# Performance work log

Hardware: AMD Instinct MI355X
Metric: run time of the kernel (lower is better)

The kernel has to match this reference:

```python
import jax, jax.numpy as jnp
import numpy as np

EPS = 1e-12  # torch F.normalize default eps


def conv1x1(x, w, b):
    # x: [N,C,H,W], w: [K,C], b: [K]
    return jnp.einsum('nchw,kc->nkhw', x, w) + b[None, :, None, None]


def forward_sa(f1, f2, cw1, cb1, cw2, cb2):
    n, _, h, w = f1.shape
    c1 = conv1x1(f1, cw1, cb1)  # [N,1,H,W]
    c2 = conv1x1(f2, cw2, cb2)
    c1 = jax.nn.softmax(c1.reshape(n, h * w), axis=1).reshape(n, 1, h, w)
    c2 = jax.nn.softmax(c2.reshape(n, h * w), axis=1).reshape(n, 1, h, w)
    return c1 * f1, c2 * f2


def l2norm_ch(x):
    # torch F.normalize(x) -> p=2 over dim=1 with eps clamp
    n = jnp.sqrt(jnp.sum(x * x, axis=1, keepdims=True))
    return x / jnp.maximum(n, EPS)


def forward_ca(f1, f2, pw1, pb1, pw2, pb2):
    N, C, H, W = f1.shape
    f1_cl = conv1x1(f1, pw1, pb1).reshape(N, -1, H * W)  # [N,Cl,HW]
    f2_cl = conv1x1(f2, pw2, pb2).reshape(N, -1, H * W)
    # A[n,p,q] = sum_c f2_cl[n,c,p] * f1_cl[n,c,q]  -> [N,HW,HW]
    A_c = jnp.tanh(jnp.einsum('ncp,ncq->npq', f2_cl, f1_cl))
    f1_v = f1.reshape(N, C, H * W)
    f2_v = f2.reshape(N, C, H * W)
    # f1_hat = f1_v @ A_c^T ; f2_hat = f2_v @ A_c
    f1_hat = jnp.einsum('ncp,nqp->ncq', f1_v, A_c).reshape(N, C, H, W)
    f2_hat = jnp.einsum('ncp,npq->ncq', f2_v, A_c).reshape(N, C, H, W)
    return l2norm_ch(f1_hat), l2norm_ch(f2_hat)


def setup_inputs() -> dict:
    key = jax.random.key(0)
    ks = jax.random.split(key, 10)
    N, C, H, W = 2, 256, 64, 64
    Cl = C // 16
    sc = 1.0 / np.sqrt(C)
    return {
        'f1': jax.random.normal(ks[0], (N, C, H, W), jnp.float32),
        'f2': jax.random.normal(ks[1], (N, C, H, W), jnp.float32),
        'pw1': jax.random.normal(ks[2], (Cl, C), jnp.float32) * sc,
        'pb1': jax.random.normal(ks[3], (Cl,), jnp.float32) * sc,
        'pw2': jax.random.normal(ks[4], (Cl, C), jnp.float32) * sc,
        'pb2': jax.random.normal(ks[5], (Cl,), jnp.float32) * sc,
        'cw1': jax.random.normal(ks[6], (1, C), jnp.float32) * sc,
        'cb1': jax.random.normal(ks[7], (1,), jnp.float32) * sc,
        'cw2': jax.random.normal(ks[8], (1, C), jnp.float32) * sc,
        'cb2': jax.random.normal(ks[9], (1,), jnp.float32) * sc,
    }


def reference(f1, f2, pw1, pb1, pw2, pb2, cw1, cb1, cw2, cb2):
    f1_1, f2_1 = forward_sa(f1, f2, cw1, cb1, cw2, cb2)
    f1_hat, f2_hat = forward_ca(f1_1, f2_1, pw1, pb1, pw2, pb2)
    fp1_hat = jax.nn.relu(f1_hat + f1)
    fp2_hat = jax.nn.relu(f2_hat + f2)
    f1_2, f2_2 = forward_sa(fp1_hat, fp2_hat, cw1, cb1, cw2, cb2)
    # Original calls forward_ca(f1_2, f2_2) again but discards the result
    # and returns (f1_2, f2_2); the dead call is omitted (identical output).
    return (f1_2, f2_2)
```

## Files before the change

kernel.cpp:

```cpp
#include <hip/hip_runtime.h>
#include <hip/hip_bf16.h>
#include <math.h>

#define N_B 2
#define C_CH 256
#define HW_SZ 4096
#define CL_CH 16

typedef __bf16 bf16x8 __attribute__((ext_vector_type(8)));
typedef float f32x4 __attribute__((ext_vector_type(4)));
typedef float f32x16 __attribute__((ext_vector_type(16)));

__device__ __forceinline__ unsigned short f2bf(float x){
  __hip_bfloat16 b = __float2bfloat16(x);
  return *reinterpret_cast<unsigned short*>(&b);
}
__device__ __forceinline__ float bf2f(unsigned short u){
  unsigned int w = ((unsigned int)u) << 16;
  return *reinterpret_cast<float*>(&w);
}
__device__ __forceinline__ unsigned int cvtpk(float a, float b){
  unsigned int r;
  asm("v_cvt_pk_bf16_f32 %0, %1, %2" : "=v"(r) : "v"(a), "v"(b));
  return r;
}
__device__ __forceinline__ float tanh_fast(float x){
  float e = __expf(2.0f * x);
  return fmaf(-2.0f, __builtin_amdgcn_rcpf(1.0f + e), 1.0f);
}
__device__ __forceinline__ void gload16(const void* gsrc, void* lds_dst){
  __builtin_amdgcn_global_load_lds(
      (const __attribute__((address_space(1))) unsigned int*)gsrc,
      (__attribute__((address_space(3))) unsigned int*)lds_dst, 16, 0, 0);
}

__global__ void k_conv1(const float* __restrict__ f1, const float* __restrict__ f2,
                        const float* __restrict__ w1, const float* __restrict__ w2,
                        const float* __restrict__ b1, const float* __restrict__ b2,
                        float* __restrict__ cv){
  const int i = blockIdx.z, n = blockIdx.y, t = threadIdx.x;
  const int ql = t & 63, cg = t >> 6;
  const int q = blockIdx.x * 64 + ql;
  const float* f = (i ? f2 : f1) + n * C_CH * HW_SZ;
  const float* w = i ? w2 : w1;
  __shared__ float ws[C_CH];
  __shared__ float red[4][72];
  ws[t] = w[t];
  __syncthreads();
  float acc = 0.f;
  #pragma unroll 8
  for (int c = cg * 64; c < cg * 64 + 64; ++c)
    acc += f[c * HW_SZ + q] * ws[c];
  red[cg][ql] = acc;
  __syncthreads();
  if (t < 64){
    float s = red[0][t] + red[1][t] + red[2][t] + red[3][t] + (i ? b2[0] : b1[0]);
    cv[(i * 2 + n) * HW_SZ + blockIdx.x * 64 + t] = s;
  }
}

__global__ void k_scale_cl(const float* __restrict__ f1, const float* __restrict__ f2,
                           const float* __restrict__ cv,
                           const float* __restrict__ pw1, const float* __restrict__ pw2,
                           const float* __restrict__ pb1, const float* __restrict__ pb2,
                           unsigned short* __restrict__ fs1, unsigned short* __restrict__ fs2,
                           unsigned short* __restrict__ clT1, unsigned short* __restrict__ clT2){
  const int i = blockIdx.z, n = blockIdx.y, t = threadIdx.x;
  const int ql = t & 63, cg = t >> 6;
  const int q = blockIdx.x * 64 + ql;
  const float* f = (i ? f2 : f1) + n * C_CH * HW_SZ;
  unsigned short* fs = (i ? fs2 : fs1) + n * C_CH * HW_SZ;
  unsigned short* clT = (i ? clT2 : clT1) + n * 32 * HW_SZ;
  const float* pw = i ? pw2 : pw1;
  const float* pb = i ? pb2 : pb1;
  const float* cvrow = cv + (i * 2 + n) * HW_SZ;
  __shared__ float wls[CL_CH * C_CH];
  __shared__ float red[4][CL_CH][66];
  __shared__ float smr[256];
  #pragma unroll
  for (int j = 0; j < 16; j++) wls[j * 256 + t] = pw[j * 256 + t];
  float sv[16];
  float m = -1e30f;
  #pragma unroll
  for (int j = 0; j < 16; j++){ sv[j] = cvrow[j * 256 + t]; m = fmaxf(m, sv[j]); }
  smr[t] = m; __syncthreads();
  for (int s = 128; s > 0; s >>= 1){ if (t < s) smr[t] = fmaxf(smr[t], smr[t + s]); __syncthreads(); }
  m = smr[0]; __syncthreads();
  float sum = 0.f;
  #pragma unroll
  for (int j = 0; j < 16; j++) sum += __expf(sv[j] - m);
  smr[t] = sum; __syncthreads();
  for (int s = 128; s > 0; s >>= 1){ if (t < s) smr[t] += smr[t + s]; __syncthreads(); }
  const float p = __expf(cvrow[q] - m) * (1.0f / smr[0]);

  float acc[16];
  #pragma unroll
  for (int k = 0; k < 16; k++) acc[k] = 0.f;
  for (int c = cg * 64; c < cg * 64 + 64; ++c){
    float vv = f[c * HW_SZ + q] * p;
    fs[c * HW_SZ + q] = f2bf(vv);
    #pragma unroll
    for (int k = 0; k < 16; k++) acc[k] += wls[k * 256 + c] * vv;
  }
  #pragma unroll
  for (int k = 0; k < 16; k++) red[cg][k][ql] = acc[k];
  __syncthreads();
  #pragma unroll
  for (int j = 0; j < 4; j++){
    int e = j * 256 + t; int k = e >> 6, qq = e & 63;
    float s = red[0][k][qq] + red[1][k][qq] + red[2][k][qq] + red[3][k][qq] + pb[k];
    clT[(blockIdx.x * 64 + qq) * 32 + k] = f2bf(s);
  }
  if (t < 128){
    uint4 zv = {0u, 0u, 0u, 0u};
    int qq = t >> 1, half = t & 1;
    *reinterpret_cast<uint4*>(&clT[(blockIdx.x * 64 + qq) * 32 + 16 + half * 8]) = zv;
  }
}

__global__ __launch_bounds__(512, 2) void k_hat(
    const unsigned short* __restrict__ fs1, const unsigned short* __restrict__ fs2,
    const unsigned short* __restrict__ clT1, const unsigned short* __restrict__ clT2,
    float* __restrict__ hat1, float* __restrict__ hat2,
    float* __restrict__ pt1, float* __restrict__ pt2){
  const int t = threadIdx.x;
  const int bid = blockIdx.x;
  const int xcd = bid & 7, slot = bid >> 3;
  const int z = xcd >> 1;
  const int n = z & 1, i = z >> 1;
  const int x = slot * 2 + (xcd & 1);
  const int qt = x >> 1, ph = x & 1;
  const int q0 = qt * 128;
  const int pbase = ph * 2048;

  const unsigned short* fs = (i ? fs2 : fs1) + n * C_CH * HW_SZ;
  const unsigned short* uT = (i ? clT1 : clT2) + n * 32 * HW_SZ;
  const unsigned short* vT = (i ? clT2 : clT1) + n * 32 * HW_SZ;
  float* out = (ph ? (i ? pt2 : pt1) : (i ? hat2 : hat1)) + n * C_CH * HW_SZ;

  __shared__ __align__(16) unsigned short fsA[2][C_CH * 64];
  __shared__ __align__(16) unsigned short aT[2][128 * 64];

  const int wv = t >> 6, l = t & 63;
  const int g4 = l >> 4, lr16 = l & 15;
  const int g2 = l >> 5, lr32 = l & 31;

  const int pfw = wv & 3;
  const int qh  = wv >> 2;
  const int cblk = wv & 3, qblk = wv >> 2;

  bf16x8 ub[4];
  #pragma unroll
  for (int j = 0; j < 4; ++j)
    ub[j] = *reinterpret_cast<const bf16x8*>(&uT[(q0 + qh * 64 + j * 16 + lr16) * 32 + g4 * 8]);

  f32x16 acc00, acc01, acc10, acc11;
  #pragma unroll
  for (int r = 0; r < 16; ++r){ acc00[r] = 0.f; acc01[r] = 0.f; acc10[r] = 0.f; acc11[r] = 0.f; }
  const f32x4 zz = {0.f, 0.f, 0.f, 0.f};

  int fs_src[4];
  #pragma unroll
  for (int it = 0; it < 4; ++it){
    int d = it * 512 + t; int c = d >> 3, sl = d & 7;
    int u = sl ^ (c & 7) ^ (((c >> 3) & 1) << 2) ^ (((c >> 4) & 1) << 1);
    fs_src[it] = c * (HW_SZ * 2) + u * 16;
  }
  const int vgo = (pfw * 16 + lr16) * 64 + g4 * 16;
  unsigned atw0;
  {
    int qd = qh * 64 + lr16;
    int sw = (pfw * 2 + (g4 >> 1)) ^ (qd & 7) ^ (((qd >> 3) & 1) << 2);
    atw0 = qd * 128 + sw * 16 + (g4 & 1) * 8;
  }
  unsigned afo[2], bqo[2];
  #pragma unroll
  for (int cf = 0; cf < 2; ++cf){
    int crow = cblk * 64 + cf * 32 + lr32;
    afo[cf] = crow * 128 +
      ((g2 ^ (crow & 7) ^ (((crow >> 3) & 1) << 2) ^ (((crow >> 4) & 1) << 1)) << 4);
  }
  #pragma unroll
  for (int qf = 0; qf < 2; ++qf){
    int qrow = qblk * 64 + qf * 32 + lr32;
    bqo[qf] = qrow * 128 +
      ((g2 ^ (qrow & 7) ^ (((qrow >> 3) & 1) << 2) ^ (((qrow >> 4) & 1) << 1)) << 4);
  }

  auto stage_fs = [&](unsigned short* dstbase, const char* src){
    #pragma unroll
    for (int it = 0; it < 4; ++it)
      gload16(src + fs_src[it], dstbase + (it * 512 + wv * 64) * 8);
  };
  auto dgen = [&](uint4 vr, char* atB){
    bf16x8 av = *reinterpret_cast<bf16x8*>(&vr);
    #pragma unroll
    for (int j = 0; j < 4; ++j){
      f32x4 d = __builtin_amdgcn_mfma_f32_16x16x32_bf16(av, ub[j], zz, 0, 0, 0);
      uint2 pk;
      pk.x = cvtpk(tanh_fast(d[0]), tanh_fast(d[1]));
      pk.y = cvtpk(tanh_fast(d[2]), tanh_fast(d[3]));
      unsigned off = (atw0 + (unsigned)(j * 2048)) ^ ((unsigned)(j & 1) << 5);
      *reinterpret_cast<uint2*>(atB + off) = pk;
    }
  };
  auto mmain = [&](const char* faB, const char* atB){
    __builtin_amdgcn_s_setprio(1);
    #pragma unroll
    for (int ks = 0; ks < 4; ++ks){
      unsigned kx = (unsigned)(ks << 5);
      bf16x8 a0 = *reinterpret_cast<const bf16x8*>(faB + (afo[0] ^ kx));
      bf16x8 a1 = *reinterpret_cast<const bf16x8*>(faB + (afo[1] ^ kx));
      bf16x8 b0 = *reinterpret_cast<const bf16x8*>(atB + (bqo[0] ^ kx));
      bf16x8 b1 = *reinterpret_cast<const bf16x8*>(atB + (bqo[1] ^ kx));
      acc00 = __builtin_amdgcn_mfma_f32_32x32x16_bf16(a0, b0, acc00, 0, 0, 0);
      acc01 = __builtin_amdgcn_mfma_f32_32x32x16_bf16(a0, b1, acc01, 0, 0, 0);
      acc10 = __builtin_amdgcn_mfma_f32_32x32x16_bf16(a1, b0, acc10, 0, 0, 0);
      acc11 = __builtin_amdgcn_mfma_f32_32x32x16_bf16(a1, b1, acc11, 0, 0, 0);
    }
    __builtin_amdgcn_s_setprio(0);
  };

  const char* fpp = (const char*)fs + pbase * 2;
  const char* vp  = (const char*)vT + pbase * 64 + vgo;

  stage_fs(fsA[0], fpp); fpp += 128;
  uint4 va = *reinterpret_cast<const uint4*>(vp);
  uint4 vb = *reinterpret_cast<const uint4*>(vp + 4096);
  vp += 8192;
  dgen(va, (char*)aT[0]);

  #pragma unroll 1
  for (int k2 = 0; k2 < 16; ++k2){
    {
      stage_fs(fsA[1], fpp); fpp += 128;
      va = *reinterpret_cast<const uint4*>(vp); vp += 4096;
      dgen(vb, (char*)aT[1]);
      asm volatile("s_waitcnt lgkmcnt(0)" ::: "memory");
      __builtin_amdgcn_sched_barrier(0);
      __builtin_amdgcn_s_barrier();
      __builtin_amdgcn_sched_barrier(0);
      mmain((const char*)fsA[0], (const char*)aT[0]);
      __builtin_amdgcn_sched_barrier(0);
      __builtin_amdgcn_s_barrier();
      __builtin_amdgcn_sched_barrier(0);
    }
    {
      stage_fs(fsA[0], fpp); fpp += 128;
      vb = *reinterpret_cast<const uint4*>(vp); vp += 4096;
      dgen(va, (char*)aT[0]);
      asm volatile("s_waitcnt lgkmcnt(0)" ::: "memory");
      __builtin_amdgcn_sched_barrier(0);
      __builtin_amdgcn_s_barrier();
      __builtin_amdgcn_sched_barrier(0);
      mmain((const char*)fsA[1], (const char*)aT[1]);
      __builtin_amdgcn_sched_barrier(0);
      __builtin_amdgcn_s_barrier();
      __builtin_amdgcn_sched_barrier(0);
    }
  }

  const int qcol = q0 + qblk * 64 + lr32;
  #pragma unroll
  for (int r = 0; r < 16; ++r){
    int cr = (r & 3) + 8 * (r >> 2) + 4 * g2;
    out[(cblk * 64 + cr) * HW_SZ + qcol] = acc00[r];
    out[(cblk * 64 + cr) * HW_SZ + qcol + 32] = acc01[r];
    out[(cblk * 64 + 32 + cr) * HW_SZ + qcol] = acc10[r];
    out[(cblk * 64 + 32 + cr) * HW_SZ + qcol + 32] = acc11[r];
  }
}

__global__ void k_norm(const float* __restrict__ hat1, const float* __restrict__ hat2,
                       const float* __restrict__ pt1, const float* __restrict__ pt2,
                       const float* __restrict__ f1, const float* __restrict__ f2,
                       const float* __restrict__ cw1, const float* __restrict__ cw2,
                       const float* __restrict__ cb1, const float* __restrict__ cb2,
                       unsigned short* __restrict__ fpb1, unsigned short* __restrict__ fpb2,
                       float* __restrict__ cv2){
  const int i = blockIdx.z, n = blockIdx.y, t = threadIdx.x;
  const int ql = t & 63, cg = t >> 6;
  const int q = blockIdx.x * 64 + ql;
  const float* hat = (i ? hat2 : hat1) + n * C_CH * HW_SZ;
  const float* pt = (i ? pt2 : pt1) + n * C_CH * HW_SZ;
  const float* f = (i ? f2 : f1) + n * C_CH * HW_SZ;
  unsigned short* fpb = (i ? fpb2 : fpb1) + n * C_CH * HW_SZ;
  __shared__ float ws[C_CH];
  __shared__ float red[4][72];
  __shared__ float invs[64];
  __shared__ unsigned short hLs[C_CH][66];
  ws[t] = (i ? cw2 : cw1)[t];
  __syncthreads();
  float s = 0.f;
  #pragma unroll 8
  for (int c = cg * 64; c < cg * 64 + 64; ++c){
    float h = hat[c * HW_SZ + q] + pt[c * HW_SZ + q];
    hLs[c][ql] = f2bf(h);
    s += h * h;
  }
  red[cg][ql] = s; __syncthreads();
  if (t < 64){
    float ss = red[0][t] + red[1][t] + red[2][t] + red[3][t];
    invs[t] = 1.0f / fmaxf(sqrtf(ss), 1e-12f);
  }
  __syncthreads();
  const float inv = invs[ql];
  float ca = 0.f;
  #pragma unroll 8
  for (int c = cg * 64; c < cg * 64 + 64; ++c){
    float vv = fmaxf(bf2f(hLs[c][ql]) * inv + f[c * HW_SZ + q], 0.0f);
    fpb[c * HW_SZ + q] = f2bf(vv);
    ca += ws[c] * vv;
  }
  red[cg][ql] = ca; __syncthreads();
  if (t < 64){
    float ss = red[0][t] + red[1][t] + red[2][t] + red[3][t] + (i ? cb2[0] : cb1[0]);
    cv2[(i * 2 + n) * HW_SZ + blockIdx.x * 64 + t] = ss;
  }
}

__global__ void k_final(const unsigned short* __restrict__ fp1,
                        const unsigned short* __restrict__ fp2,
                        const float* __restrict__ cv2, float* __restrict__ outp){
  const int i = blockIdx.z, t = threadIdx.x;
  const int idx4 = (blockIdx.x * 256 + t) * 4;
  const int n = idx4 >> 20;
  const int q = idx4 & (HW_SZ - 1);
  const float* cvrow = cv2 + (i * 2 + n) * HW_SZ;
  __shared__ float red[256];
  float sv[16];
  float m = -1e30f;
  #pragma unroll
  for (int j = 0; j < 16; j++){ sv[j] = cvrow[j * 256 + t]; m = fmaxf(m, sv[j]); }
  red[t] = m; __syncthreads();
  for (int s = 128; s > 0; s >>= 1){ if (t < s) red[t] = fmaxf(red[t], red[t + s]); __syncthreads(); }
  m = red[0]; __syncthreads();
  float sum = 0.f;
  #pragma unroll
  for (int j = 0; j < 16; j++) sum += __expf(sv[j] - m);
  red[t] = sum; __syncthreads();
  for (int s = 128; s > 0; s >>= 1){ if (t < s) red[t] += red[t + s]; __syncthreads(); }
  const float invS = 1.0f / red[0];

  const unsigned short* fp = i ? fp2 : fp1;
  ushort4 vv = *reinterpret_cast<const ushort4*>(&fp[idx4]);
  float4 o;
  o.x = bf2f(vv.x) * (__expf(cvrow[q + 0] - m) * invS);
  o.y = bf2f(vv.y) * (__expf(cvrow[q + 1] - m) * invS);
  o.z = bf2f(vv.z) * (__expf(cvrow[q + 2] - m) * invS);
  o.w = bf2f(vv.w) * (__expf(cvrow[q + 3] - m) * invS);
  *reinterpret_cast<float4*>(&outp[i * (C_CH * HW_SZ * N_B) + idx4]) = o;
}

extern "C" void kernel_launch(void* const* d_in, const int* in_sizes, int n_in,
                              void* d_out, int out_size, void* d_ws, size_t ws_size,
                              hipStream_t stream){
  const float* f1  = (const float*)d_in[0];
  const float* f2  = (const float*)d_in[1];
  const float* pw1 = (const float*)d_in[2];
  const float* pb1 = (const float*)d_in[3];
  const float* pw2 = (const float*)d_in[4];
  const float* pb2 = (const float*)d_in[5];
  const float* cw1 = (const float*)d_in[6];
  const float* cb1 = (const float*)d_in[7];
  const float* cw2 = (const float*)d_in[8];
  const float* cb2 = (const float*)d_in[9];
  float* ws = (float*)d_ws;
  float* HAT1 = ws;
  float* HAT2 = ws + 2097152;
  float* PT1  = ws + 4194304;
  float* PT2  = ws + 6291456;
  unsigned short* FS1 = (unsigned short*)(ws + 8388608);
  unsigned short* FS2 = (unsigned short*)(ws + 9437184);
  unsigned short* CLT1 = (unsigned short*)(ws + 10485760);
  unsigned short* CLT2 = (unsigned short*)(ws + 10616832);
  float* CV1  = ws + 10747904;
  float* CV2  = ws + 10764288;
  float* outp = (float*)d_out;
  unsigned short* FPB1 = FS1;
  unsigned short* FPB2 = FS2;

  k_conv1   <<<dim3(64, 2, 2), 256, 0, stream>>>(f1, f2, cw1, cw2, cb1, cb2, CV1);
  k_scale_cl<<<dim3(64, 2, 2), 256, 0, stream>>>(f1, f2, CV1, pw1, pw2, pb1, pb2,
                                                 FS1, FS2, CLT1, CLT2);
  k_hat     <<<256, 512, 0, stream>>>(FS1, FS2, CLT1, CLT2, HAT1, HAT2, PT1, PT2);
  k_norm    <<<dim3(64, 2, 2), 256, 0, stream>>>(HAT1, HAT2, PT1, PT2, f1, f2,
                                                 cw1, cw2, cb1, cb2, FPB1, FPB2, CV2);
  k_final   <<<dim3(2048, 1, 2), 256, 0, stream>>>(FPB1, FPB2, CV2, outp);
}
```

Measured before the change: 97.26 us.

## Triple-buffer LDS tiles to drop the trailing barrier per K step

Raises the shared-memory staging of the feature tile and the tanh attention tile from two buffers to three, rotating read/write/spare pointers. That removes the second workgroup barrier after each MFMA phase, since the buffer being written is never the one just read. The cost is about 50% more LDS per block (about 144KB). This could lower occupancy, or even exceed the LDS limit depending on the hardware's per-CU capacity.

```diff
diff --git a/kernel.cpp b/kernel.cpp
--- a/kernel.cpp
+++ b/kernel.cpp
@@ -138,8 +138,8 @@
   const unsigned short* vT = (i ? clT2 : clT1) + n * 32 * HW_SZ;
   float* out = (ph ? (i ? pt2 : pt1) : (i ? hat2 : hat1)) + n * C_CH * HW_SZ;
 
-  __shared__ __align__(16) unsigned short fsA[2][C_CH * 64];
-  __shared__ __align__(16) unsigned short aT[2][128 * 64];
+  __shared__ __align__(16) unsigned short fsA[3][C_CH * 64];
+  __shared__ __align__(16) unsigned short aT[3][128 * 64];
 
   const int wv = t >> 6, l = t & 63;
   const int g4 = l >> 4, lr16 = l & 15;
@@ -187,10 +187,10 @@
       ((g2 ^ (qrow & 7) ^ (((qrow >> 3) & 1) << 2) ^ (((qrow >> 4) & 1) << 1)) << 4);
   }
 
-  auto stage_fs = [&](unsigned short* dstbase, const char* src){
+  auto stage_fs = [&](char* dstbase, const char* src){
     #pragma unroll
     for (int it = 0; it < 4; ++it)
-      gload16(src + fs_src[it], dstbase + (it * 512 + wv * 64) * 8);
+      gload16(src + fs_src[it], dstbase + (it * 512 + wv * 64) * 16);
   };
   auto dgen = [&](uint4 vr, char* atB){
     bf16x8 av = *reinterpret_cast<bf16x8*>(&vr);
@@ -224,40 +224,31 @@
   const char* fpp = (const char*)fs + pbase * 2;
   const char* vp  = (const char*)vT + pbase * 64 + vgo;
 
-  stage_fs(fsA[0], fpp); fpp += 128;
-  uint4 va = *reinterpret_cast<const uint4*>(vp);
-  uint4 vb = *reinterpret_cast<const uint4*>(vp + 4096);
-  vp += 8192;
-  dgen(va, (char*)aT[0]);
+  char *fRd = (char*)&fsA[0][0], *fWr = (char*)&fsA[1][0], *fSp = (char*)&fsA[2][0];
+  char *aRd = (char*)&aT[0][0],  *aWr = (char*)&aT[1][0],  *aSp = (char*)&aT[2][0];
+
+  stage_fs(fRd, fpp); fpp += 128;
+  uint4 vb;
+  {
+    uint4 va = *reinterpret_cast<const uint4*>(vp);
+    vb = *reinterpret_cast<const uint4*>(vp + 4096);
+    vp += 8192;
+    dgen(va, aRd);
+  }
 
   #pragma unroll 1
-  for (int k2 = 0; k2 < 16; ++k2){
-    {
-      stage_fs(fsA[1], fpp); fpp += 128;
-      va = *reinterpret_cast<const uint4*>(vp); vp += 4096;
-      dgen(vb, (char*)aT[1]);
-      asm volatile("s_waitcnt lgkmcnt(0)" ::: "memory");
-      __builtin_amdgcn_sched_barrier(0);
-      __builtin_amdgcn_s_barrier();
-      __builtin_amdgcn_sched_barrier(0);
-      mmain((const char*)fsA[0], (const char*)aT[0]);
-      __builtin_amdgcn_sched_barrier(0);
-      __builtin_amdgcn_s_barrier();
-      __builtin_amdgcn_sched_barrier(0);
-    }
-    {
-      stage_fs(fsA[0], fpp); fpp += 128;
-      vb = *reinterpret_cast<const uint4*>(vp); vp += 4096;
-      dgen(va, (char*)aT[0]);
-      asm volatile("s_waitcnt lgkmcnt(0)" ::: "memory");
-      __builtin_amdgcn_sched_barrier(0);
-      __builtin_amdgcn_s_barrier();
-      __builtin_amdgcn_sched_barrier(0);
-      mmain((const char*)fsA[1], (const char*)aT[1]);
-      __builtin_amdgcn_sched_barrier(0);
-      __builtin_amdgcn_s_barrier();
-      __builtin_amdgcn_sched_barrier(0);
-    }
+  for (int k = 0; k < 32; ++k){
+    stage_fs(fWr, fpp); fpp += 128;
+    uint4 vnew = *reinterpret_cast<const uint4*>(vp); vp += 4096;
+    dgen(vb, aWr);
+    vb = vnew;
+    asm volatile("s_waitcnt lgkmcnt(0)" ::: "memory");
+    __builtin_amdgcn_sched_barrier(0);
+    __builtin_amdgcn_s_barrier();
+    __builtin_amdgcn_sched_barrier(0);
+    mmain(fRd, aRd);
+    char* tf = fRd; fRd = fWr; fWr = fSp; fSp = tf;
+    char* ta = aRd; aRd = aWr; aWr = aSp; aSp = ta;
   }
 
   const int qcol = q0 + qblk * 64 + lr32;
```

Measured after the change: 96.72 us. No clear change (-0.6%).
